# Kernel optimization log

Measured on AMD Instinct MI355X. Metric: run time of the kernel, lower is better.

## Reference

```python
import jax, jax.numpy as jnp
import numpy as np

N = 100000      # nodes
E = 1600000     # edges (avg degree 16)
EL = 200000     # supervision (label) edges
D_IN, D_HID, D_OUT = 128, 128, 64


def setup_inputs() -> dict:
    key = jax.random.key(0)
    k = jax.random.split(key, 6)
    x = jax.random.normal(k[0], (N, D_IN), jnp.float32)
    edge_index = jax.random.randint(k[1], (2, E), 0, N, dtype=jnp.int32)
    edge_label_index = jax.random.randint(k[2], (2, EL), 0, N, dtype=jnp.int32)
    W1 = jax.random.normal(k[3], (D_IN, D_HID), jnp.float32) * (1.0 / np.sqrt(D_IN))
    b1 = jnp.zeros((D_HID,), jnp.float32)
    W2 = jax.random.normal(k[4], (D_HID, D_OUT), jnp.float32) * (1.0 / np.sqrt(D_HID))
    b2 = jnp.zeros((D_OUT,), jnp.float32)
    return {"x": x, "edge_index": edge_index, "edge_label_index": edge_label_index,
            "W1": W1, "b1": b1, "W2": W2, "b2": b2}


def gcn_layer(x, src, dst, W, b, n):
    """PyG-style GCNConv: linear -> sym-normalized scatter-add with self loops -> +bias."""
    h = x @ W                                   # [N, F]
    ones = jnp.ones(src.shape[0], h.dtype)
    deg = jax.ops.segment_sum(ones, dst, num_segments=n) + 1.0   # in-degree + self loop
    dinv = jax.lax.rsqrt(deg)                   # deg^{-1/2}
    norm = dinv[src] * dinv[dst]                # per-edge norm
    agg = jax.ops.segment_sum(h[src] * norm[:, None], dst, num_segments=n)
    agg = agg + h * (1.0 / deg)[:, None]        # self-loop contribution: dinv[i]^2
    return agg + b


def reference(x, edge_index, edge_label_index, W1, b1, W2, b2):
    src, dst = edge_index[0], edge_index[1]
    z = gcn_layer(x, src, dst, W1, b1, N)
    z = jax.nn.relu(z)                          # dropout omitted (eval mode)
    z = gcn_layer(z, src, dst, W2, b2, N)
    # decode: gather-dot over supervision edges
    return (z[edge_label_index[0]] * z[edge_label_index[1]]).sum(axis=-1)
```

## Files before the change

### kernel.cpp

```cpp
#include <hip/hip_runtime.h>
#include <stdint.h>

typedef __bf16 bf16x8 __attribute__((ext_vector_type(8)));
typedef float  floatx4 __attribute__((ext_vector_type(4)));

__device__ __forceinline__ unsigned short f2b(float x){
    unsigned u = __float_as_uint(x);
    u = u + 0x7FFFu + ((u >> 16) & 1u);
    return (unsigned short)(u >> 16);
}
__device__ __forceinline__ float b2f(unsigned short h){
    return __uint_as_float(((unsigned)h) << 16);
}


__global__ __launch_bounds__(256) void k_hist(const int* __restrict__ dst,
                                              int* __restrict__ hist,
                                              int E_, int nbins, int nblk){
    __shared__ int h[1024];
    int t = threadIdx.x, blk = blockIdx.x;
    for (int i = t; i < nbins; i += 256) h[i] = 0;
    __syncthreads();
    int base = blk * 8192;
    #pragma unroll
    for (int j = 0; j < 8; j++){
        int e = base + (j * 256 + t) * 4;
        if (e < E_){
            int4 d = *(const int4*)(dst + e);
            atomicAdd(&h[d.x >> 7], 1);
            atomicAdd(&h[d.y >> 7], 1);
            atomicAdd(&h[d.z >> 7], 1);
            atomicAdd(&h[d.w >> 7], 1);
        }
    }
    __syncthreads();
    for (int i = t; i < nbins; i += 256) hist[(size_t)i * nblk + blk] = h[i];
}

__global__ __launch_bounds__(64) void k_binscanA(int* __restrict__ hist,
                                                 int* __restrict__ btot, int nblk){
    int bin = blockIdx.x, lane = threadIdx.x;
    int carry = 0;
    for (int base = 0; base < nblk; base += 64){
        int idx = bin * nblk + base + lane;
        bool inb = (base + lane) < nblk;
        int v = inb ? hist[idx] : 0;
        int orig = v;
        #pragma unroll
        for (int o = 1; o < 64; o <<= 1){
            int u = __shfl_up(v, o);
            if (lane >= o) v += u;
        }
        if (inb) hist[idx] = v - orig + carry;
        carry += __shfl(v, 63);
    }
    if (lane == 0) btot[bin] = carry;
}

__global__ __launch_bounds__(1024) void k_binscanB(const int* __restrict__ btot,
                                                   int* __restrict__ boff, int nbins){
    __shared__ int s[1024];
    int t = threadIdx.x;
    s[t] = (t < nbins) ? btot[t] : 0;
    __syncthreads();
    for (int o = 1; o < 1024; o <<= 1){
        int v = (t >= o) ? s[t - o] : 0;
        __syncthreads();
        s[t] += v;
        __syncthreads();
    }
    if (t == 0) boff[0] = 0;
    if (t < nbins) boff[t + 1] = s[t];
}

__global__ __launch_bounds__(256) void k_scatter(const int* __restrict__ src,
                                                 const int* __restrict__ dst,
                                                 const int* __restrict__ hist,
                                                 const int* __restrict__ boff,
                                                 unsigned* __restrict__ part,
                                                 int E_, int nbins, int nblk){
    __shared__ int cur[1024];
    int t = threadIdx.x, blk = blockIdx.x;
    for (int i = t; i < nbins; i += 256)
        cur[i] = boff[i] + hist[(size_t)i * nblk + blk];
    __syncthreads();
    int base = blk * 8192;
    #pragma unroll
    for (int j = 0; j < 8; j++){
        int e = base + (j * 256 + t) * 4;
        if (e < E_){
            int4 d = *(const int4*)(dst + e);
            int4 s = *(const int4*)(src + e);
            int p0 = atomicAdd(&cur[d.x >> 7], 1);
            part[p0] = ((unsigned)(d.x & 127) << 25) | (unsigned)s.x;
            int p1 = atomicAdd(&cur[d.y >> 7], 1);
            part[p1] = ((unsigned)(d.y & 127) << 25) | (unsigned)s.y;
            int p2 = atomicAdd(&cur[d.z >> 7], 1);
            part[p2] = ((unsigned)(d.z & 127) << 25) | (unsigned)s.z;
            int p3 = atomicAdd(&cur[d.w >> 7], 1);
            part[p3] = ((unsigned)(d.w & 127) << 25) | (unsigned)s.w;
        }
    }
}

__global__ __launch_bounds__(256) void k_binsort(const unsigned* __restrict__ part,
                                                 const int* __restrict__ boff,
                                                 int* __restrict__ csr,
                                                 int* __restrict__ cnt,
                                                 int* __restrict__ off,
                                                 float* __restrict__ dinv,
                                                 int n, int nbins){
    int b = blockIdx.x, t = threadIdx.x;
    int s0 = boff[b], s1 = boff[b + 1], len = s1 - s0;
    __shared__ int cl[128], sc[128], cur[128];
    __shared__ unsigned buf[4096], outb[4096];
    if (t < 128){ cl[t] = 0; cur[t] = 0; }
    __syncthreads();
    if (len <= 4096){
        for (int i = t; i < len; i += 256) buf[i] = part[s0 + i];
        __syncthreads();
        for (int i = t; i < len; i += 256) atomicAdd(&cl[buf[i] >> 25], 1);
        __syncthreads();
        if (t < 128) sc[t] = cl[t];
        __syncthreads();
        for (int o = 1; o < 128; o <<= 1){
            int v = 0;
            if (t < 128 && t >= o) v = sc[t - o];
            __syncthreads();
            if (t < 128) sc[t] += v;
            __syncthreads();
        }
        for (int i = t; i < len; i += 256){
            unsigned w = buf[i];
            int nd = (int)(w >> 25);
            int p = (sc[nd] - cl[nd]) + atomicAdd(&cur[nd], 1);
            outb[p] = w & 0x1FFFFFFu;
        }
        __syncthreads();
        for (int i = t; i < len; i += 256) csr[s0 + i] = (int)outb[i];
    } else {
        for (int i = t; i < len; i += 256) atomicAdd(&cl[part[s0 + i] >> 25], 1);
        __syncthreads();
        if (t < 128) sc[t] = cl[t];
        __syncthreads();
        for (int o = 1; o < 128; o <<= 1){
            int v = 0;
            if (t < 128 && t >= o) v = sc[t - o];
            __syncthreads();
            if (t < 128) sc[t] += v;
            __syncthreads();
        }
        for (int i = t; i < len; i += 256){
            unsigned w = part[s0 + i];
            int nd = (int)(w >> 25);
            int p = (sc[nd] - cl[nd]) + atomicAdd(&cur[nd], 1);
            csr[s0 + p] = (int)(w & 0x1FFFFFFu);
        }
    }
    if (t < 128){
        int node = b * 128 + t;
        if (node < n){
            cnt[node] = cl[t];
            off[node] = s0 + (sc[t] - cl[t]);
            dinv[node] = rsqrtf((float)cl[t] + 1.0f);
        }
    }
}

__global__ __launch_bounds__(256) void k_wconv(const float* __restrict__ W1,
                                               const float* __restrict__ W2,
                                               unsigned short* __restrict__ wf1,
                                               unsigned short* __restrict__ wf2){
    int f = blockIdx.x * 256 + threadIdx.x;
    if (f >= 3072) return;
    const float* W; unsigned short* o; int ncol, lf;
    if (f < 2048){ W = W1; o = wf1; ncol = 128; lf = f; }
    else         { W = W2; o = wf2; ncol = 64;  lf = f - 2048; }
    int lane = lf & 63;
    int ctkc = lf >> 6;
    int kc = ctkc & 3, ct = ctkc >> 2;
    int col = ct * 16 + (lane & 15);
    int k0  = kc * 32 + (lane >> 4) * 8;
    unsigned short* d = o + (size_t)lf * 8;
    #pragma unroll
    for (int j = 0; j < 8; j++) d[j] = f2b(W[(k0 + j) * ncol + col]);
}

__global__ __launch_bounds__(256) void k_gemm1(const float* __restrict__ x,
                                               const unsigned short* __restrict__ wf,
                                               const float* __restrict__ dinv,
                                               unsigned short* __restrict__ hs, int n){
    __shared__ unsigned short Wl[16384];
    __shared__ unsigned short Al[64 * 136];
    int t = threadIdx.x;
    long rowBase = (long)blockIdx.x * 64;
    {
        const uint4* s4 = (const uint4*)wf;
        uint4* d4 = (uint4*)Wl;
        #pragma unroll
        for (int i = 0; i < 8; i++) d4[t + i * 256] = s4[t + i * 256];
    }
    {
        const float4* xs = (const float4*)(x + rowBase * 128);
        #pragma unroll
        for (int k = 0; k < 8; k++){
            int i = t + k * 256;
            int r = i >> 5, c4 = (i & 31) << 2;
            float4 v = make_float4(0.f, 0.f, 0.f, 0.f);
            if (rowBase + r < n) v = xs[i];
            unsigned lo = (unsigned)f2b(v.x) | ((unsigned)f2b(v.y) << 16);
            unsigned hi = (unsigned)f2b(v.z) | ((unsigned)f2b(v.w) << 16);
            *(uint2*)&Al[r * 136 + c4] = make_uint2(lo, hi);
        }
    }
    __syncthreads();
    int w = t >> 6, lane = t & 63, lr = lane & 15, q = lane >> 4;
    floatx4 zero = {0.f, 0.f, 0.f, 0.f};
    floatx4 acc[8];
    #pragma unroll
    for (int ct = 0; ct < 8; ct++) acc[ct] = zero;
    #pragma unroll
    for (int kc = 0; kc < 4; kc++){
        bf16x8 af = *(const bf16x8*)&Al[(w * 16 + lr) * 136 + kc * 32 + q * 8];
        #pragma unroll
        for (int ct = 0; ct < 8; ct++){
            bf16x8 bf = *(const bf16x8*)&Wl[((ct * 4 + kc) * 64 + lane) * 8];
            acc[ct] = __builtin_amdgcn_mfma_f32_16x16x32_bf16(af, bf, acc[ct], 0, 0, 0);
        }
    }
    long r0 = rowBase + w * 16 + q * 4;
    #pragma unroll
    for (int r = 0; r < 4; r++){
        long row = r0 + r;
        if (row >= n) continue;
        float dv = dinv[row];
        unsigned short* orow = hs + row * 128 + lr;
        #pragma unroll
        for (int ct = 0; ct < 8; ct++) orow[ct * 16] = f2b(acc[ct][r] * dv);
    }
}

__global__ __launch_bounds__(256) void k_gemm2(const unsigned short* __restrict__ z1,
                                               const unsigned short* __restrict__ wf,
                                               const float* __restrict__ dinv,
                                               unsigned short* __restrict__ hs, int n){
    __shared__ unsigned short Wl[8192];
    __shared__ unsigned short Al[64 * 136];
    int t = threadIdx.x;
    long rowBase = (long)blockIdx.x * 64;
    {
        const uint4* s4 = (const uint4*)wf;
        uint4* d4 = (uint4*)Wl;
        #pragma unroll
        for (int i = 0; i < 4; i++) d4[t + i * 256] = s4[t + i * 256];
    }
    {
        const uint4* zs = (const uint4*)(z1 + rowBase * 128);
        #pragma unroll
        for (int k = 0; k < 4; k++){
            int i = t + k * 256;
            int r = i >> 4, c8 = (i & 15) << 3;
            uint4 v = make_uint4(0u, 0u, 0u, 0u);
            if (rowBase + r < n) v = zs[i];
            *(uint4*)&Al[r * 136 + c8] = v;
        }
    }
    __syncthreads();
    int w = t >> 6, lane = t & 63, lr = lane & 15, q = lane >> 4;
    floatx4 zero = {0.f, 0.f, 0.f, 0.f};
    floatx4 acc[4];
    #pragma unroll
    for (int ct = 0; ct < 4; ct++) acc[ct] = zero;
    #pragma unroll
    for (int kc = 0; kc < 4; kc++){
        bf16x8 af = *(const bf16x8*)&Al[(w * 16 + lr) * 136 + kc * 32 + q * 8];
        #pragma unroll
        for (int ct = 0; ct < 4; ct++){
            bf16x8 bf = *(const bf16x8*)&Wl[((ct * 4 + kc) * 64 + lane) * 8];
            acc[ct] = __builtin_amdgcn_mfma_f32_16x16x32_bf16(af, bf, acc[ct], 0, 0, 0);
        }
    }
    long r0 = rowBase + w * 16 + q * 4;
    #pragma unroll
    for (int r = 0; r < 4; r++){
        long row = r0 + r;
        if (row >= n) continue;
        float dv = dinv[row];
        unsigned short* orow = hs + row * 64 + lr;
        #pragma unroll
        for (int ct = 0; ct < 4; ct++) orow[ct * 16] = f2b(acc[ct][r] * dv);
    }
}

__global__ __launch_bounds__(256) void k_agg1(const unsigned short* __restrict__ hs,
                                              const int* __restrict__ off,
                                              const int* __restrict__ cnt,
                                              const int* __restrict__ csr,
                                              const float* __restrict__ dinv,
                                              const float* __restrict__ b,
                                              unsigned short* __restrict__ z, int n){
    int wid = (blockIdx.x * 256 + threadIdx.x) >> 6;
    int lane = threadIdx.x & 63;
    if (wid >= n) return;
    size_t i = (size_t)wid;
    int start = off[wid], c = cnt[wid];
    unsigned v0 = *(const unsigned*)(hs + i * 128 + lane * 2);
    float a0 = b2f((unsigned short)v0);
    float a1 = b2f((unsigned short)(v0 >> 16));
    int j = 0;
    for (; j + 8 <= c; j += 8){
        size_t s0 = (size_t)csr[start + j + 0];
        size_t s1 = (size_t)csr[start + j + 1];
        size_t s2 = (size_t)csr[start + j + 2];
        size_t s3 = (size_t)csr[start + j + 3];
        size_t s4 = (size_t)csr[start + j + 4];
        size_t s5 = (size_t)csr[start + j + 5];
        size_t s6 = (size_t)csr[start + j + 6];
        size_t s7 = (size_t)csr[start + j + 7];
        unsigned w0 = *(const unsigned*)(hs + s0 * 128 + lane * 2);
        unsigned w1 = *(const unsigned*)(hs + s1 * 128 + lane * 2);
        unsigned w2 = *(const unsigned*)(hs + s2 * 128 + lane * 2);
        unsigned w3 = *(const unsigned*)(hs + s3 * 128 + lane * 2);
        unsigned w4 = *(const unsigned*)(hs + s4 * 128 + lane * 2);
        unsigned w5 = *(const unsigned*)(hs + s5 * 128 + lane * 2);
        unsigned w6 = *(const unsigned*)(hs + s6 * 128 + lane * 2);
        unsigned w7 = *(const unsigned*)(hs + s7 * 128 + lane * 2);
        a0 += b2f((unsigned short)w0); a1 += b2f((unsigned short)(w0 >> 16));
        a0 += b2f((unsigned short)w1); a1 += b2f((unsigned short)(w1 >> 16));
        a0 += b2f((unsigned short)w2); a1 += b2f((unsigned short)(w2 >> 16));
        a0 += b2f((unsigned short)w3); a1 += b2f((unsigned short)(w3 >> 16));
        a0 += b2f((unsigned short)w4); a1 += b2f((unsigned short)(w4 >> 16));
        a0 += b2f((unsigned short)w5); a1 += b2f((unsigned short)(w5 >> 16));
        a0 += b2f((unsigned short)w6); a1 += b2f((unsigned short)(w6 >> 16));
        a0 += b2f((unsigned short)w7); a1 += b2f((unsigned short)(w7 >> 16));
    }
    for (; j < c; j++){
        size_t s = (size_t)csr[start + j];
        unsigned v = *(const unsigned*)(hs + s * 128 + lane * 2);
        a0 += b2f((unsigned short)v);
        a1 += b2f((unsigned short)(v >> 16));
    }
    float dv = dinv[wid];
    float2 bb = ((const float2*)b)[lane];
    float z0 = fmaxf(fmaf(dv, a0, bb.x), 0.f);
    float z1 = fmaxf(fmaf(dv, a1, bb.y), 0.f);
    *(unsigned*)(z + i * 128 + lane * 2) = (unsigned)f2b(z0) | ((unsigned)f2b(z1) << 16);
}

__global__ __launch_bounds__(256) void k_agg2(const unsigned short* __restrict__ hs,
                                              const int* __restrict__ off,
                                              const int* __restrict__ cnt,
                                              const int* __restrict__ csr,
                                              const float* __restrict__ dinv,
                                              const float* __restrict__ b,
                                              float* __restrict__ z, int n){
    int wid = (blockIdx.x * 256 + threadIdx.x) >> 6;
    int lane = threadIdx.x & 63;
    if (wid >= n) return;
    size_t i = (size_t)wid;
    int start = off[wid], c = cnt[wid];
    float a = b2f(hs[i * 64 + lane]);
    int j = 0;
    for (; j + 8 <= c; j += 8){
        size_t s0 = (size_t)csr[start + j + 0];
        size_t s1 = (size_t)csr[start + j + 1];
        size_t s2 = (size_t)csr[start + j + 2];
        size_t s3 = (size_t)csr[start + j + 3];
        size_t s4 = (size_t)csr[start + j + 4];
        size_t s5 = (size_t)csr[start + j + 5];
        size_t s6 = (size_t)csr[start + j + 6];
        size_t s7 = (size_t)csr[start + j + 7];
        unsigned short h0 = hs[s0 * 64 + lane];
        unsigned short h1 = hs[s1 * 64 + lane];
        unsigned short h2 = hs[s2 * 64 + lane];
        unsigned short h3 = hs[s3 * 64 + lane];
        unsigned short h4 = hs[s4 * 64 + lane];
        unsigned short h5 = hs[s5 * 64 + lane];
        unsigned short h6 = hs[s6 * 64 + lane];
        unsigned short h7 = hs[s7 * 64 + lane];
        a += b2f(h0); a += b2f(h1); a += b2f(h2); a += b2f(h3);
        a += b2f(h4); a += b2f(h5); a += b2f(h6); a += b2f(h7);
    }
    for (; j < c; j++){
        size_t s = (size_t)csr[start + j];
        a += b2f(hs[s * 64 + lane]);
    }
    z[i * 64 + lane] = fmaf(dinv[wid], a, b[lane]);
}

__global__ __launch_bounds__(256) void k_decode(const float* __restrict__ z,
                                                const int* __restrict__ es,
                                                const int* __restrict__ et,
                                                float* __restrict__ out, int m){
    int wv = (blockIdx.x * 256 + threadIdx.x) >> 6;
    int lane = threadIdx.x & 63;
    int e = wv * 2 + (lane >> 5);
    int hl = lane & 31;
    float p = 0.f;
    if (e < m){
        size_t s = (size_t)es[e], t2 = (size_t)et[e];
        float2 xs = *(const float2*)(z + s * 64 + hl * 2);
        float2 xt = *(const float2*)(z + t2 * 64 + hl * 2);
        p = xs.x * xt.x + xs.y * xt.y;
    }
    #pragma unroll
    for (int o = 16; o > 0; o >>= 1) p += __shfl_xor(p, o);
    if (hl == 0 && e < m) out[e] = p;
}


extern "C" void kernel_launch(void* const* d_in, const int* in_sizes, int n_in,
                              void* d_out, int out_size, void* d_ws, size_t ws_size,
                              hipStream_t stream){
    const float* x   = (const float*)d_in[0];
    const int*   ei  = (const int*)d_in[1];
    const int*   eli = (const int*)d_in[2];
    const float* W1  = (const float*)d_in[3];
    const float* b1  = (const float*)d_in[4];
    const float* W2  = (const float*)d_in[5];
    const float* b2  = (const float*)d_in[6];
    float* out = (float*)d_out;

    int N_  = in_sizes[0] / 128;
    int E_  = in_sizes[1] / 2;
    int EL_ = in_sizes[2] / 2;
    int NBINS = (N_ + 127) >> 7;
    const int EPB = 8192;
    int NBLK = (E_ + EPB - 1) / EPB;

    char* w = (char*)d_ws;
    size_t o = 0;
    auto alloc = [&](size_t bytes) -> size_t {
        size_t r = o; o += (bytes + 511) & ~(size_t)511; return r;
    };
    size_t o_cnt  = alloc((size_t)N_ * 4);
    size_t o_off  = alloc((size_t)N_ * 4);
    size_t o_dinv = alloc((size_t)N_ * 4);
    size_t o_btot = alloc((size_t)NBINS * 4);
    size_t o_boff = alloc((size_t)(NBINS + 1) * 4);
    size_t o_csr  = alloc((size_t)E_ * 4);
    size_t o_wf1  = alloc(16384 * 2);
    size_t o_wf2  = alloc(8192 * 2);
    size_t o_hs1  = alloc((size_t)N_ * 128 * 2);
    size_t o_z1   = alloc((size_t)N_ * 128 * 2);

    int* cnt  = (int*)(w + o_cnt);
    int* off  = (int*)(w + o_off);
    float* dinv = (float*)(w + o_dinv);
    int* btot = (int*)(w + o_btot);
    int* boff = (int*)(w + o_boff);
    int* csr  = (int*)(w + o_csr);
    unsigned short* wf1 = (unsigned short*)(w + o_wf1);
    unsigned short* wf2 = (unsigned short*)(w + o_wf2);
    unsigned short* hs1 = (unsigned short*)(w + o_hs1);
    unsigned short* z1  = (unsigned short*)(w + o_z1);
    unsigned short* hs2 = hs1;
    float* z2 = (float*)(w + o_z1);

    int* hist = (int*)(w + o_hs1);
    unsigned* part = (unsigned*)(w + o_hs1 + 4u * 1024u * 1024u);

    k_hist    <<<NBLK, 256, 0, stream>>>(ei + E_, hist, E_, NBINS, NBLK);
    k_binscanA<<<NBINS, 64, 0, stream>>>(hist, btot, NBLK);
    k_binscanB<<<1, 1024, 0, stream>>>(btot, boff, NBINS);
    k_scatter <<<NBLK, 256, 0, stream>>>(ei, ei + E_, hist, boff, part, E_, NBINS, NBLK);
    k_binsort <<<NBINS, 256, 0, stream>>>(part, boff, csr, cnt, off, dinv, N_, NBINS);
    k_wconv   <<<12, 256, 0, stream>>>(W1, W2, wf1, wf2);
    k_gemm1   <<<(N_ + 63) / 64, 256, 0, stream>>>(x, wf1, dinv, hs1, N_);
    k_agg1    <<<(N_ + 3) / 4, 256, 0, stream>>>(hs1, off, cnt, csr, dinv, b1, z1, N_);
    k_gemm2   <<<(N_ + 63) / 64, 256, 0, stream>>>(z1, wf2, dinv, hs2, N_);
    k_agg2    <<<(N_ + 3) / 4, 256, 0, stream>>>(hs2, off, cnt, csr, dinv, b2, z2, N_);
    k_decode  <<<(EL_ + 7) / 8, 256, 0, stream>>>(z2, eli, eli + EL_, out, EL_);
}
```

Measured before the change: 317.4 us.

## Fuse layer-1 aggregation with layer-2 GEMM in a persistent kernel

Merges the first-layer aggregation (with bias and ReLU) and the second-layer linear transform into one persistent kernel. Each wave aggregates a node, stages the 128-wide row in LDS and multiplies by W2, which is held in LDS as fp32, so the bf16 z1 intermediate is never written to or read from global memory. The final layer output is also stored as bf16 instead of fp32 to halve decode gather traffic. The tradeoff is that the MFMA GEMM becomes a scalar fp32 FMA loop per node (128 FMAs per lane), the 32KB of LDS limits occupancy, and the fixed grid of 1024 blocks may underfill the device, while bf16 output loses some precision.

```diff
diff --git a/kernel.cpp b/kernel.cpp
--- a/kernel.cpp
+++ b/kernel.cpp
@@ -168,22 +168,17 @@
 }
 
 __global__ __launch_bounds__(256) void k_wconv(const float* __restrict__ W1,
-                                               const float* __restrict__ W2,
-                                               unsigned short* __restrict__ wf1,
-                                               unsigned short* __restrict__ wf2){
-    int f = blockIdx.x * 256 + threadIdx.x;
-    if (f >= 3072) return;
-    const float* W; unsigned short* o; int ncol, lf;
-    if (f < 2048){ W = W1; o = wf1; ncol = 128; lf = f; }
-    else         { W = W2; o = wf2; ncol = 64;  lf = f - 2048; }
+                                               unsigned short* __restrict__ wf1){
+    int lf = blockIdx.x * 256 + threadIdx.x;
+    if (lf >= 2048) return;
     int lane = lf & 63;
     int ctkc = lf >> 6;
     int kc = ctkc & 3, ct = ctkc >> 2;
     int col = ct * 16 + (lane & 15);
     int k0  = kc * 32 + (lane >> 4) * 8;
-    unsigned short* d = o + (size_t)lf * 8;
-    #pragma unroll
-    for (int j = 0; j < 8; j++) d[j] = f2b(W[(k0 + j) * ncol + col]);
+    unsigned short* d = wf1 + (size_t)lf * 8;
+    #pragma unroll
+    for (int j = 0; j < 8; j++) d[j] = f2b(W1[(k0 + j) * 128 + col]);
 }
 
 __global__ __launch_bounds__(256) void k_gemm1(const float* __restrict__ x,
@@ -240,120 +235,86 @@
     }
 }
 
-__global__ __launch_bounds__(256) void k_gemm2(const unsigned short* __restrict__ z1,
-                                               const unsigned short* __restrict__ wf,
-                                               const float* __restrict__ dinv,
-                                               unsigned short* __restrict__ hs, int n){
-    __shared__ unsigned short Wl[8192];
-    __shared__ unsigned short Al[64 * 136];
+__global__ __launch_bounds__(256) void k_agg1g2(const unsigned short* __restrict__ hs,
+                                                const int* __restrict__ off,
+                                                const int* __restrict__ cnt,
+                                                const int* __restrict__ csr,
+                                                const float* __restrict__ dinv,
+                                                const float* __restrict__ b1,
+                                                const float* __restrict__ W2,
+                                                unsigned short* __restrict__ hs2,
+                                                int n, int nwaves){
+    __shared__ float W2l[128 * 64];
+    __shared__ float zrow[4][128];
     int t = threadIdx.x;
-    long rowBase = (long)blockIdx.x * 64;
     {
-        const uint4* s4 = (const uint4*)wf;
-        uint4* d4 = (uint4*)Wl;
-        #pragma unroll
-        for (int i = 0; i < 4; i++) d4[t + i * 256] = s4[t + i * 256];
-    }
-    {
-        const uint4* zs = (const uint4*)(z1 + rowBase * 128);
-        #pragma unroll
-        for (int k = 0; k < 4; k++){
-            int i = t + k * 256;
-            int r = i >> 4, c8 = (i & 15) << 3;
-            uint4 v = make_uint4(0u, 0u, 0u, 0u);
-            if (rowBase + r < n) v = zs[i];
-            *(uint4*)&Al[r * 136 + c8] = v;
-        }
-    }
-    __syncthreads();
-    int w = t >> 6, lane = t & 63, lr = lane & 15, q = lane >> 4;
-    floatx4 zero = {0.f, 0.f, 0.f, 0.f};
-    floatx4 acc[4];
-    #pragma unroll
-    for (int ct = 0; ct < 4; ct++) acc[ct] = zero;
-    #pragma unroll
-    for (int kc = 0; kc < 4; kc++){
-        bf16x8 af = *(const bf16x8*)&Al[(w * 16 + lr) * 136 + kc * 32 + q * 8];
-        #pragma unroll
-        for (int ct = 0; ct < 4; ct++){
-            bf16x8 bf = *(const bf16x8*)&Wl[((ct * 4 + kc) * 64 + lane) * 8];
-            acc[ct] = __builtin_amdgcn_mfma_f32_16x16x32_bf16(af, bf, acc[ct], 0, 0, 0);
-        }
-    }
-    long r0 = rowBase + w * 16 + q * 4;
-    #pragma unroll
-    for (int r = 0; r < 4; r++){
-        long row = r0 + r;
-        if (row >= n) continue;
-        float dv = dinv[row];
-        unsigned short* orow = hs + row * 64 + lr;
-        #pragma unroll
-        for (int ct = 0; ct < 4; ct++) orow[ct * 16] = f2b(acc[ct][r] * dv);
-    }
-}
-
-__global__ __launch_bounds__(256) void k_agg1(const unsigned short* __restrict__ hs,
+        const float4* w4 = (const float4*)W2;
+        float4* d4 = (float4*)W2l;
+        #pragma unroll
+        for (int i = 0; i < 8; i++) d4[t + i * 256] = w4[t + i * 256];
+    }
+    __syncthreads();
+    int wband = t >> 6, lane = t & 63;
+    float2 bb = ((const float2*)b1)[lane];
+    for (int wid = blockIdx.x * 4 + wband; wid < n; wid += nwaves){
+        size_t i = (size_t)wid;
+        int start = off[wid], c = cnt[wid];
+        unsigned v0 = *(const unsigned*)(hs + i * 128 + lane * 2);
+        float a0 = b2f((unsigned short)v0);
+        float a1 = b2f((unsigned short)(v0 >> 16));
+        int j = 0;
+        for (; j + 8 <= c; j += 8){
+            size_t s0 = (size_t)csr[start + j + 0];
+            size_t s1 = (size_t)csr[start + j + 1];
+            size_t s2 = (size_t)csr[start + j + 2];
+            size_t s3 = (size_t)csr[start + j + 3];
+            size_t s4 = (size_t)csr[start + j + 4];
+            size_t s5 = (size_t)csr[start + j + 5];
+            size_t s6 = (size_t)csr[start + j + 6];
+            size_t s7 = (size_t)csr[start + j + 7];
+            unsigned w0 = *(const unsigned*)(hs + s0 * 128 + lane * 2);
+            unsigned w1 = *(const unsigned*)(hs + s1 * 128 + lane * 2);
+            unsigned w2 = *(const unsigned*)(hs + s2 * 128 + lane * 2);
+            unsigned w3 = *(const unsigned*)(hs + s3 * 128 + lane * 2);
+            unsigned w4 = *(const unsigned*)(hs + s4 * 128 + lane * 2);
+            unsigned w5 = *(const unsigned*)(hs + s5 * 128 + lane * 2);
+            unsigned w6 = *(const unsigned*)(hs + s6 * 128 + lane * 2);
+            unsigned w7 = *(const unsigned*)(hs + s7 * 128 + lane * 2);
+            a0 += b2f((unsigned short)w0); a1 += b2f((unsigned short)(w0 >> 16));
+            a0 += b2f((unsigned short)w1); a1 += b2f((unsigned short)(w1 >> 16));
+            a0 += b2f((unsigned short)w2); a1 += b2f((unsigned short)(w2 >> 16));
+            a0 += b2f((unsigned short)w3); a1 += b2f((unsigned short)(w3 >> 16));
+            a0 += b2f((unsigned short)w4); a1 += b2f((unsigned short)(w4 >> 16));
+            a0 += b2f((unsigned short)w5); a1 += b2f((unsigned short)(w5 >> 16));
+            a0 += b2f((unsigned short)w6); a1 += b2f((unsigned short)(w6 >> 16));
+            a0 += b2f((unsigned short)w7); a1 += b2f((unsigned short)(w7 >> 16));
+        }
+        for (; j < c; j++){
+            size_t s = (size_t)csr[start + j];
+            unsigned v = *(const unsigned*)(hs + s * 128 + lane * 2);
+            a0 += b2f((unsigned short)v);
+            a1 += b2f((unsigned short)(v >> 16));
+        }
+        float dv = dinv[wid];
+        float z0 = fmaxf(fmaf(dv, a0, bb.x), 0.f);
+        float z1 = fmaxf(fmaf(dv, a1, bb.y), 0.f);
+        zrow[wband][lane * 2]     = z0;
+        zrow[wband][lane * 2 + 1] = z1;
+        float acc = 0.f;
+        #pragma unroll 16
+        for (int k = 0; k < 128; k++)
+            acc = fmaf(zrow[wband][k], W2l[k * 64 + lane], acc);
+        hs2[i * 64 + lane] = f2b(acc * dv);
+    }
+}
+
+__global__ __launch_bounds__(256) void k_agg2(const unsigned short* __restrict__ hs,
                                               const int* __restrict__ off,
                                               const int* __restrict__ cnt,
                                               const int* __restrict__ csr,
                                               const float* __restrict__ dinv,
                                               const float* __restrict__ b,
                                               unsigned short* __restrict__ z, int n){
-    int wid = (blockIdx.x * 256 + threadIdx.x) >> 6;
-    int lane = threadIdx.x & 63;
-    if (wid >= n) return;
-    size_t i = (size_t)wid;
-    int start = off[wid], c = cnt[wid];
-    unsigned v0 = *(const unsigned*)(hs + i * 128 + lane * 2);
-    float a0 = b2f((unsigned short)v0);
-    float a1 = b2f((unsigned short)(v0 >> 16));
-    int j = 0;
-    for (; j + 8 <= c; j += 8){
-        size_t s0 = (size_t)csr[start + j + 0];
-        size_t s1 = (size_t)csr[start + j + 1];
-        size_t s2 = (size_t)csr[start + j + 2];
-        size_t s3 = (size_t)csr[start + j + 3];
-        size_t s4 = (size_t)csr[start + j + 4];
-        size_t s5 = (size_t)csr[start + j + 5];
-        size_t s6 = (size_t)csr[start + j + 6];
-        size_t s7 = (size_t)csr[start + j + 7];
-        unsigned w0 = *(const unsigned*)(hs + s0 * 128 + lane * 2);
-        unsigned w1 = *(const unsigned*)(hs + s1 * 128 + lane * 2);
-        unsigned w2 = *(const unsigned*)(hs + s2 * 128 + lane * 2);
-        unsigned w3 = *(const unsigned*)(hs + s3 * 128 + lane * 2);
-        unsigned w4 = *(const unsigned*)(hs + s4 * 128 + lane * 2);
-        unsigned w5 = *(const unsigned*)(hs + s5 * 128 + lane * 2);
-        unsigned w6 = *(const unsigned*)(hs + s6 * 128 + lane * 2);
-        unsigned w7 = *(const unsigned*)(hs + s7 * 128 + lane * 2);
-        a0 += b2f((unsigned short)w0); a1 += b2f((unsigned short)(w0 >> 16));
-        a0 += b2f((unsigned short)w1); a1 += b2f((unsigned short)(w1 >> 16));
-        a0 += b2f((unsigned short)w2); a1 += b2f((unsigned short)(w2 >> 16));
-        a0 += b2f((unsigned short)w3); a1 += b2f((unsigned short)(w3 >> 16));
-        a0 += b2f((unsigned short)w4); a1 += b2f((unsigned short)(w4 >> 16));
-        a0 += b2f((unsigned short)w5); a1 += b2f((unsigned short)(w5 >> 16));
-        a0 += b2f((unsigned short)w6); a1 += b2f((unsigned short)(w6 >> 16));
-        a0 += b2f((unsigned short)w7); a1 += b2f((unsigned short)(w7 >> 16));
-    }
-    for (; j < c; j++){
-        size_t s = (size_t)csr[start + j];
-        unsigned v = *(const unsigned*)(hs + s * 128 + lane * 2);
-        a0 += b2f((unsigned short)v);
-        a1 += b2f((unsigned short)(v >> 16));
-    }
-    float dv = dinv[wid];
-    float2 bb = ((const float2*)b)[lane];
-    float z0 = fmaxf(fmaf(dv, a0, bb.x), 0.f);
-    float z1 = fmaxf(fmaf(dv, a1, bb.y), 0.f);
-    *(unsigned*)(z + i * 128 + lane * 2) = (unsigned)f2b(z0) | ((unsigned)f2b(z1) << 16);
-}
-
-__global__ __launch_bounds__(256) void k_agg2(const unsigned short* __restrict__ hs,
-                                              const int* __restrict__ off,
-                                              const int* __restrict__ cnt,
-                                              const int* __restrict__ csr,
-                                              const float* __restrict__ dinv,
-                                              const float* __restrict__ b,
-                                              float* __restrict__ z, int n){
     int wid = (blockIdx.x * 256 + threadIdx.x) >> 6;
     int lane = threadIdx.x & 63;
     if (wid >= n) return;
@@ -385,10 +346,10 @@
         size_t s = (size_t)csr[start + j];
         a += b2f(hs[s * 64 + lane]);
     }
-    z[i * 64 + lane] = fmaf(dinv[wid], a, b[lane]);
-}
-
-__global__ __launch_bounds__(256) void k_decode(const float* __restrict__ z,
+    z[i * 64 + lane] = f2b(fmaf(dinv[wid], a, b[lane]));
+}
+
+__global__ __launch_bounds__(256) void k_decode(const unsigned short* __restrict__ z,
                                                 const int* __restrict__ es,
                                                 const int* __restrict__ et,
                                                 float* __restrict__ out, int m){
@@ -399,9 +360,10 @@
     float p = 0.f;
     if (e < m){
         size_t s = (size_t)es[e], t2 = (size_t)et[e];
-        float2 xs = *(const float2*)(z + s * 64 + hl * 2);
-        float2 xt = *(const float2*)(z + t2 * 64 + hl * 2);
-        p = xs.x * xt.x + xs.y * xt.y;
+        unsigned vs = *(const unsigned*)(z + s * 64 + hl * 2);
+        unsigned vt = *(const unsigned*)(z + t2 * 64 + hl * 2);
+        p = b2f((unsigned short)vs) * b2f((unsigned short)vt)
+          + b2f((unsigned short)(vs >> 16)) * b2f((unsigned short)(vt >> 16));
     }
     #pragma unroll
     for (int o = 16; o > 0; o >>= 1) p += __shfl_xor(p, o);
@@ -440,9 +402,8 @@
     size_t o_boff = alloc((size_t)(NBINS + 1) * 4);
     size_t o_csr  = alloc((size_t)E_ * 4);
     size_t o_wf1  = alloc(16384 * 2);
-    size_t o_wf2  = alloc(8192 * 2);
     size_t o_hs1  = alloc((size_t)N_ * 128 * 2);
-    size_t o_z1   = alloc((size_t)N_ * 128 * 2);
+    size_t o_hs2  = alloc((size_t)N_ * 64 * 2);
 
     int* cnt  = (int*)(w + o_cnt);
     int* off  = (int*)(w + o_off);
@@ -451,24 +412,24 @@
     int* boff = (int*)(w + o_boff);
     int* csr  = (int*)(w + o_csr);
     unsigned short* wf1 = (unsigned short*)(w + o_wf1);
-    unsigned short* wf2 = (unsigned short*)(w + o_wf2);
     unsigned short* hs1 = (unsigned short*)(w + o_hs1);
-    unsigned short* z1  = (unsigned short*)(w + o_z1);
-    unsigned short* hs2 = hs1;
-    float* z2 = (float*)(w + o_z1);
+    unsigned short* hs2 = (unsigned short*)(w + o_hs2);
+    unsigned short* z2  = (unsigned short*)(w + o_hs1);
 
     int* hist = (int*)(w + o_hs1);
     unsigned* part = (unsigned*)(w + o_hs1 + 4u * 1024u * 1024u);
+
+    const int AGG1_BLOCKS = 1024;
+    int nwaves = AGG1_BLOCKS * 4;
 
     k_hist    <<<NBLK, 256, 0, stream>>>(ei + E_, hist, E_, NBINS, NBLK);
     k_binscanA<<<NBINS, 64, 0, stream>>>(hist, btot, NBLK);
     k_binscanB<<<1, 1024, 0, stream>>>(btot, boff, NBINS);
     k_scatter <<<NBLK, 256, 0, stream>>>(ei, ei + E_, hist, boff, part, E_, NBINS, NBLK);
     k_binsort <<<NBINS, 256, 0, stream>>>(part, boff, csr, cnt, off, dinv, N_, NBINS);
-    k_wconv   <<<12, 256, 0, stream>>>(W1, W2, wf1, wf2);
+    k_wconv   <<<8, 256, 0, stream>>>(W1, wf1);
     k_gemm1   <<<(N_ + 63) / 64, 256, 0, stream>>>(x, wf1, dinv, hs1, N_);
-    k_agg1    <<<(N_ + 3) / 4, 256, 0, stream>>>(hs1, off, cnt, csr, dinv, b1, z1, N_);
-    k_gemm2   <<<(N_ + 63) / 64, 256, 0, stream>>>(z1, wf2, dinv, hs2, N_);
+    k_agg1g2  <<<AGG1_BLOCKS, 256, 0, stream>>>(hs1, off, cnt, csr, dinv, b1, W2, hs2, N_, nwaves);
     k_agg2    <<<(N_ + 3) / 4, 256, 0, stream>>>(hs2, off, cnt, csr, dinv, b2, z2, N_);
     k_decode  <<<(EL_ + 7) / 8, 256, 0, stream>>>(z2, eli, eli + EL_, out, EL_);
 }
```

Measured after the change: 365.4 us. +15.1%, slower.
